# Kernel optimization log

Hardware: AMD Instinct MI355X
Metric: run time of the kernel (lower is better)

## Reference

```python
import jax, jax.numpy as jnp
import numpy as np

COUT, CIN = 1024, 1024  # self.shape = (cout, cin) in the torch module
NNZ = 131072


def setup_inputs() -> dict:
    key = jax.random.key(0)
    k_x, k_v, k_r, k_c = jax.random.split(key, 4)
    x = jax.random.normal(k_x, (4, 4096, CIN), dtype=jnp.float32)
    values = jax.random.normal(k_v, (NNZ,), dtype=jnp.float32)
    rows = jax.random.randint(k_r, (NNZ,), 0, COUT, dtype=jnp.int32)
    cols = jax.random.randint(k_c, (NNZ,), 0, CIN, dtype=jnp.int32)
    indices = jnp.stack([rows, cols], axis=0)  # [2, nnz], integer-valued
    return {"x": x, "values": values, "indices": indices}


def reference(x, values, indices):
    # torch: sparse_coo_tensor(indices, values, (cout, cin)).coalesce();
    # coalescing sums duplicate (row, col) entries -> scatter-add densify.
    rows, cols = indices[0], indices[1]
    W = jnp.zeros((COUT, CIN), dtype=values.dtype).at[rows, cols].add(values)
    # 3D path: out[b, l, co] = sum_ci W[co, ci] * x[b, l, ci]
    return jnp.einsum('blc,oc->blo', x, W)
```

## Files before the change

kernel.cpp:

```cpp
#include <hip/hip_runtime.h>
#include <cstdint>
#include <cstddef>

#define CIN  1024
#define COUT 1024

typedef __attribute__((ext_vector_type(8))) short bf16x8;
typedef __attribute__((ext_vector_type(4))) float f32x4;

__device__ __forceinline__ unsigned short f2bf(float f) {
    union { float f; unsigned int i; } v;
    v.f = f;
    unsigned int u = v.i;
    u += 0x7FFFu + ((u >> 16) & 1u);
    return (unsigned short)(u >> 16);
}

__global__ void zero_f32(float4* __restrict__ p) {
    p[blockIdx.x * 256 + threadIdx.x] = float4{0.f, 0.f, 0.f, 0.f};
}

__global__ void scatter_add(const float* __restrict__ vals,
                            const int* __restrict__ rows,
                            const int* __restrict__ cols,
                            float* __restrict__ W, int nnz) {
    int i = blockIdx.x * 256 + threadIdx.x;
    if (i < nnz) {
        atomicAdd(W + (size_t)rows[i] * CIN + cols[i], vals[i]);
    }
}

__global__ void cvt_bf16_bulk(const float* __restrict__ src, unsigned short* __restrict__ dst) {
    size_t i = ((size_t)blockIdx.x * 256 + threadIdx.x) * 8;
    float4 v0 = *(const float4*)(src + i);
    float4 v1 = *(const float4*)(src + i + 4);
    union { bf16x8 v; unsigned short u[8]; } w;
    w.u[0] = f2bf(v0.x); w.u[1] = f2bf(v0.y); w.u[2] = f2bf(v0.z); w.u[3] = f2bf(v0.w);
    w.u[4] = f2bf(v1.x); w.u[5] = f2bf(v1.y); w.u[6] = f2bf(v1.z); w.u[7] = f2bf(v1.w);
    *(bf16x8*)(dst + i) = w.v;
}

__global__ __launch_bounds__(256) void gemm_bt_bf16_sw(
    const unsigned short* __restrict__ A,
    const unsigned short* __restrict__ B,
    float* __restrict__ C,
    int M) {
    constexpr int K = CIN;
    constexpr int N = COUT;

    __shared__ __align__(16) unsigned short As[128 * 64];
    __shared__ __align__(16) unsigned short Bs[128 * 64];

    const int tid   = threadIdx.x;
    const int lane  = tid & 63;
    const int wave  = tid >> 6;
    const int waveM = (wave >> 1) * 64;
    const int waveN = (wave & 1) * 64;
    const int quad  = lane >> 4;
    const int l16   = lane & 15;

    const int rowA0 = blockIdx.x * 128;
    const int rowB0 = blockIdx.y * 128;

    const int stg_r  = tid >> 3;
    const int c_slot = tid & 7;
    const int c_data = c_slot ^ (stg_r & 7);
    const unsigned short* pa = A + (size_t)(rowA0 + stg_r) * K + c_data * 8;
    const unsigned short* pb = B + (size_t)(rowB0 + stg_r) * K + c_data * 8;
    const int ldsoff = tid * 8;

    f32x4 acc[4][4] = {};

    for (int k0 = 0; k0 < K; k0 += 64) {
#pragma unroll
        for (int it = 0; it < 4; ++it) {
            __builtin_amdgcn_global_load_lds(
                (const __attribute__((address_space(1))) void*)(pa + k0 + (size_t)it * 32 * K),
                (__attribute__((address_space(3))) void*)(As + it * 2048 + ldsoff),
                16, 0, 0);
            __builtin_amdgcn_global_load_lds(
                (const __attribute__((address_space(1))) void*)(pb + k0 + (size_t)it * 32 * K),
                (__attribute__((address_space(3))) void*)(Bs + it * 2048 + ldsoff),
                16, 0, 0);
        }
        __syncthreads();

        const int s7 = l16 & 7;
#pragma unroll
        for (int ks = 0; ks < 2; ++ks) {
            bf16x8 af[4], bfr[4];
            const int cx = ((ks * 4 + quad) ^ s7) * 8;
#pragma unroll
            for (int t = 0; t < 4; ++t) {
                af[t]  = *(const bf16x8*)(As + (waveM + t * 16 + l16) * 64 + cx);
                bfr[t] = *(const bf16x8*)(Bs + (waveN + t * 16 + l16) * 64 + cx);
            }
#pragma unroll
            for (int i = 0; i < 4; ++i)
#pragma unroll
                for (int j = 0; j < 4; ++j)
                    acc[i][j] = __builtin_amdgcn_mfma_f32_16x16x32_bf16(
                        af[i], bfr[j], acc[i][j], 0, 0, 0);
        }
        __syncthreads();
    }

#pragma unroll
    for (int i = 0; i < 4; ++i) {
#pragma unroll
        for (int r = 0; r < 4; ++r) {
            const int row = rowA0 + waveM + i * 16 + quad * 4 + r;
            float* cp = C + (size_t)row * N + rowB0 + waveN + l16;
#pragma unroll
            for (int j = 0; j < 4; ++j)
                cp[j * 16] = acc[i][j][r];
        }
    }
}

extern "C" void kernel_launch(void* const* d_in, const int* in_sizes, int n_in,
                              void* d_out, int out_size, void* d_ws, size_t ws_size,
                              hipStream_t stream) {
    const float* x    = (const float*)d_in[0];
    const float* vals = (const float*)d_in[1];
    const int*   idx  = (const int*)d_in[2];

    float* out = (float*)d_out;

    const int nnz = in_sizes[2] / 2;
    const int M   = in_sizes[0] / CIN;

    const size_t wf_bytes = (size_t)COUT * CIN * sizeof(float);
    const size_t wb_bytes = (size_t)COUT * CIN * sizeof(unsigned short);

    float*          Wf = (float*)d_ws;
    unsigned short* Wb = (unsigned short*)((char*)d_ws + wf_bytes);
    unsigned short* Xb = (unsigned short*)((char*)d_ws + wf_bytes + wb_bytes);

    zero_f32<<<dim3(COUT * CIN / (256 * 4)), dim3(256), 0, stream>>>((float4*)Wf);
    scatter_add<<<dim3((nnz + 255) / 256), dim3(256), 0, stream>>>(vals, idx, idx + nnz, Wf, nnz);
    cvt_bf16_bulk<<<dim3(COUT * CIN / (256 * 8)), dim3(256), 0, stream>>>(Wf, Wb);
    cvt_bf16_bulk<<<dim3((unsigned)((size_t)M * CIN / (256 * 8))), dim3(256), 0, stream>>>(x, Xb);
    gemm_bt_bf16_sw<<<dim3(M / 128, COUT / 128), dim3(256), 0, stream>>>(Xb, Wb, out, M);
}
```

Baseline: 161.7 us.

## Rewrite GEMM as 256x256 tile, 8-wave, double-buffered 8-phase pipelined kernel

Replaces the single-buffered 128x128 four-wave GEMM with a 256x256 tile computed by 8 waves. Each k-step is split into eight quadrant phases that interleave async global-to-LDS loads with MFMA work, using raw barriers, explicit vmcnt waits and setprio. Larger tiles raise data reuse per LDS load, and the double buffering hides memory latency behind compute. The cost is 128KB of LDS per block, fewer blocks (64 over the grid), and fragile hand-tuned waitcnt logic.

```diff
diff --git a/kernel.cpp b/kernel.cpp
--- a/kernel.cpp
+++ b/kernel.cpp
@@ -40,82 +40,132 @@
     *(bf16x8*)(dst + i) = w.v;
 }
 
-__global__ __launch_bounds__(256) void gemm_bt_bf16_sw(
+
+#define GLD16(SRC_, DST_)                                                     \
+  __builtin_amdgcn_global_load_lds(                                           \
+      (const __attribute__((address_space(1))) void*)(SRC_),                  \
+      (__attribute__((address_space(3))) void*)(DST_), 16, 0, 0)
+
+#define STAGE_A(BUF_, HALF_, KT_) do {                                        \
+    GLD16(pa + (size_t)((HALF_) * 128)      * CIN + (size_t)(KT_) * 64,       \
+          As + (BUF_) * 16384 + ((HALF_) * 128) * 64 + tid8);                 \
+    GLD16(pa + (size_t)((HALF_) * 128 + 64) * CIN + (size_t)(KT_) * 64,       \
+          As + (BUF_) * 16384 + ((HALF_) * 128 + 64) * 64 + tid8);            \
+  } while (0)
+
+#define STAGE_B(BUF_, HALF_, KT_) do {                                        \
+    GLD16(pb + (size_t)((HALF_) * 128)      * CIN + (size_t)(KT_) * 64,       \
+          Bs + (BUF_) * 16384 + ((HALF_) * 128) * 64 + tid8);                 \
+    GLD16(pb + (size_t)((HALF_) * 128 + 64) * CIN + (size_t)(KT_) * 64,       \
+          Bs + (BUF_) * 16384 + ((HALF_) * 128 + 64) * 64 + tid8);            \
+  } while (0)
+
+#define PHASE(BUF_, QA_, QB_, STAGE_BODY_, CKPT_BODY_) do {                   \
+    bf16x8 af[2][4];                                                          \
+    bf16x8 bfr[2][2];                                                         \
+    const unsigned short* abase_ =                                            \
+        As + (BUF_) * 16384 + ((QA_) * 128 + wm64) * 64;                      \
+    const unsigned short* bbase_ =                                            \
+        Bs + (BUF_) * 16384 + ((QB_) * 128 + wn32) * 64;                      \
+    _Pragma("unroll")                                                         \
+    for (int ks_ = 0; ks_ < 2; ++ks_) {                                       \
+      const int cx_ = ((ks_ * 4 + quad) ^ s7) * 8;                            \
+      _Pragma("unroll")                                                       \
+      for (int mf_ = 0; mf_ < 4; ++mf_)                                       \
+        af[ks_][mf_] = *(const bf16x8*)(abase_ + (mf_ * 16 + l16) * 64 + cx_);\
+      _Pragma("unroll")                                                       \
+      for (int nf_ = 0; nf_ < 2; ++nf_)                                       \
+        bfr[ks_][nf_] = *(const bf16x8*)(bbase_ + (nf_ * 16 + l16) * 64 + cx_);\
+    }                                                                         \
+    STAGE_BODY_                                                               \
+    __builtin_amdgcn_s_barrier();                                             \
+    asm volatile("s_waitcnt lgkmcnt(0)" ::: "memory");                        \
+    __builtin_amdgcn_sched_barrier(0);                                        \
+    __builtin_amdgcn_s_setprio(1);                                            \
+    _Pragma("unroll")                                                         \
+    for (int ks_ = 0; ks_ < 2; ++ks_)                                         \
+      _Pragma("unroll")                                                       \
+      for (int mf_ = 0; mf_ < 4; ++mf_)                                       \
+        _Pragma("unroll")                                                     \
+        for (int nf_ = 0; nf_ < 2; ++nf_)                                     \
+          acc[QA_][QB_][mf_][nf_] = __builtin_amdgcn_mfma_f32_16x16x32_bf16(  \
+              af[ks_][mf_], bfr[ks_][nf_], acc[QA_][QB_][mf_][nf_], 0, 0, 0); \
+    __builtin_amdgcn_s_setprio(0);                                            \
+    CKPT_BODY_                                                                \
+    __builtin_amdgcn_s_barrier();                                             \
+  } while (0)
+
+__global__ __launch_bounds__(512, 2) void gemm_8ph(
     const unsigned short* __restrict__ A,
     const unsigned short* __restrict__ B,
     float* __restrict__ C,
     int M) {
+    (void)M;
     constexpr int K = CIN;
-    constexpr int N = COUT;
 
-    __shared__ __align__(16) unsigned short As[128 * 64];
-    __shared__ __align__(16) unsigned short Bs[128 * 64];
+    __shared__ __align__(16) unsigned short As[2 * 16384];
+    __shared__ __align__(16) unsigned short Bs[2 * 16384];
 
-    const int tid   = threadIdx.x;
-    const int lane  = tid & 63;
-    const int wave  = tid >> 6;
-    const int waveM = (wave >> 1) * 64;
-    const int waveN = (wave & 1) * 64;
-    const int quad  = lane >> 4;
-    const int l16   = lane & 15;
+    const int tid  = threadIdx.x;
+    const int lane = tid & 63;
+    const int w    = tid >> 6;
+    const int quad = lane >> 4;
+    const int l16  = lane & 15;
+    const int s7   = l16 & 7;
+    const int wm64 = (w >> 2) * 64;
+    const int wn32 = (w & 3) * 32;
 
-    const int rowA0 = blockIdx.x * 128;
-    const int rowB0 = blockIdx.y * 128;
+    const int rowA0 = blockIdx.x * 256;
+    const int rowB0 = blockIdx.y * 256;
 
-    const int stg_r  = tid >> 3;
-    const int c_slot = tid & 7;
-    const int c_data = c_slot ^ (stg_r & 7);
-    const unsigned short* pa = A + (size_t)(rowA0 + stg_r) * K + c_data * 8;
-    const unsigned short* pb = B + (size_t)(rowB0 + stg_r) * K + c_data * 8;
-    const int ldsoff = tid * 8;
+    const int stg_row = tid >> 3;
+    const int c_data  = (tid & 7) ^ (stg_row & 7);
+    const int tid8    = tid * 8;
+    const unsigned short* pa = A + (size_t)(rowA0 + stg_row) * K + c_data * 8;
+    const unsigned short* pb = B + (size_t)(rowB0 + stg_row) * K + c_data * 8;
 
-    f32x4 acc[4][4] = {};
+    f32x4 acc[2][2][4][2] = {};
 
-    for (int k0 = 0; k0 < K; k0 += 64) {
-#pragma unroll
-        for (int it = 0; it < 4; ++it) {
-            __builtin_amdgcn_global_load_lds(
-                (const __attribute__((address_space(1))) void*)(pa + k0 + (size_t)it * 32 * K),
-                (__attribute__((address_space(3))) void*)(As + it * 2048 + ldsoff),
-                16, 0, 0);
-            __builtin_amdgcn_global_load_lds(
-                (const __attribute__((address_space(1))) void*)(pb + k0 + (size_t)it * 32 * K),
-                (__attribute__((address_space(3))) void*)(Bs + it * 2048 + ldsoff),
-                16, 0, 0);
-        }
-        __syncthreads();
+    STAGE_A(0, 0, 0); STAGE_A(0, 1, 0); STAGE_B(0, 0, 0); STAGE_B(0, 1, 0);
+    STAGE_A(1, 0, 1); STAGE_B(1, 0, 1);
+    asm volatile("s_waitcnt vmcnt(4)" ::: "memory");
+    __builtin_amdgcn_s_barrier();
 
-        const int s7 = l16 & 7;
-#pragma unroll
-        for (int ks = 0; ks < 2; ++ks) {
-            bf16x8 af[4], bfr[4];
-            const int cx = ((ks * 4 + quad) ^ s7) * 8;
-#pragma unroll
-            for (int t = 0; t < 4; ++t) {
-                af[t]  = *(const bf16x8*)(As + (waveM + t * 16 + l16) * 64 + cx);
-                bfr[t] = *(const bf16x8*)(Bs + (waveN + t * 16 + l16) * 64 + cx);
-            }
-#pragma unroll
-            for (int i = 0; i < 4; ++i)
-#pragma unroll
-                for (int j = 0; j < 4; ++j)
-                    acc[i][j] = __builtin_amdgcn_mfma_f32_16x16x32_bf16(
-                        af[i], bfr[j], acc[i][j], 0, 0, 0);
-        }
-        __syncthreads();
+#pragma unroll 1
+    for (int i = 0; i < 8; ++i) {
+        const int  k1 = 2 * i + 1;
+        const int  k2 = 2 * i + 2;
+        const int  k3 = 2 * i + 3;
+        const bool nl = (i < 7);
+
+        PHASE(0, 0, 0, STAGE_A(1, 1, k1); STAGE_B(1, 1, k1); , );
+        PHASE(0, 0, 1, , );
+        PHASE(0, 1, 0, if (nl) STAGE_A(0, 0, k2); , );
+        PHASE(0, 1, 1, if (nl) STAGE_B(0, 0, k2); ,
+              if (nl) { asm volatile("s_waitcnt vmcnt(4)" ::: "memory"); }
+              else    { asm volatile("s_waitcnt vmcnt(0)" ::: "memory"); } );
+        PHASE(1, 0, 0, if (nl) { STAGE_A(0, 1, k2); STAGE_B(0, 1, k2); } , );
+        PHASE(1, 0, 1, , );
+        PHASE(1, 1, 0, if (nl) STAGE_A(1, 0, k3); , );
+        PHASE(1, 1, 1, if (nl) STAGE_B(1, 0, k3); ,
+              if (nl) { asm volatile("s_waitcnt vmcnt(4)" ::: "memory"); } );
     }
 
 #pragma unroll
-    for (int i = 0; i < 4; ++i) {
+    for (int qa = 0; qa < 2; ++qa)
 #pragma unroll
-        for (int r = 0; r < 4; ++r) {
-            const int row = rowA0 + waveM + i * 16 + quad * 4 + r;
-            float* cp = C + (size_t)row * N + rowB0 + waveN + l16;
+        for (int qb = 0; qb < 2; ++qb)
 #pragma unroll
-            for (int j = 0; j < 4; ++j)
-                cp[j * 16] = acc[i][j][r];
-        }
-    }
+            for (int mf = 0; mf < 4; ++mf)
+#pragma unroll
+                for (int nf = 0; nf < 2; ++nf) {
+                    const int row0 = rowA0 + qa * 128 + wm64 + mf * 16 + quad * 4;
+                    float* cp = C + (size_t)row0 * COUT
+                                  + rowB0 + qb * 128 + wn32 + nf * 16 + l16;
+#pragma unroll
+                    for (int r = 0; r < 4; ++r)
+                        cp[(size_t)r * COUT] = acc[qa][qb][mf][nf][r];
+                }
 }
 
 extern "C" void kernel_launch(void* const* d_in, const int* in_sizes, int n_in,
@@ -141,5 +191,5 @@
     scatter_add<<<dim3((nnz + 255) / 256), dim3(256), 0, stream>>>(vals, idx, idx + nnz, Wf, nnz);
     cvt_bf16_bulk<<<dim3(COUT * CIN / (256 * 8)), dim3(256), 0, stream>>>(Wf, Wb);
     cvt_bf16_bulk<<<dim3((unsigned)((size_t)M * CIN / (256 * 8))), dim3(256), 0, stream>>>(x, Xb);
-    gemm_bt_bf16_sw<<<dim3(M / 128, COUT / 128), dim3(256), 0, stream>>>(Xb, Wb, out, M);
+    gemm_8ph<<<dim3(M / 256, COUT / 256), dim3(512), 0, stream>>>(Xb, Wb, out, M);
 }
```

After: 165.1 us. +2.1%, slower.

## Double-buffer GEMM with BK=32 stages and 256x128 tiles on 512-thread blocks

Applied to the files above, without the earlier changes.

Replaces the single-buffered BK=64 GEMM with a double-buffered BK=32 pipeline. The next K-slice is loaded into LDS via global_load_lds while MFMAs run on the current buffer, so each K step needs one barrier instead of two. The block tile grows to 256x128 with 8 waves (each still 64x64), and the XOR swizzle is adapted to 32-wide rows. This aims to hide global-load latency behind compute, at the cost of more LDS per block and a smaller grid.

```diff
diff --git a/kernel.cpp b/kernel.cpp
--- a/kernel.cpp
+++ b/kernel.cpp
@@ -40,82 +40,103 @@
     *(bf16x8*)(dst + i) = w.v;
 }
 
-__global__ __launch_bounds__(256) void gemm_bt_bf16_sw(
+
+#define GLD16(SRC_, DST_)                                                     \
+  __builtin_amdgcn_global_load_lds(                                           \
+      (const __attribute__((address_space(1))) void*)(SRC_),                  \
+      (__attribute__((address_space(3))) void*)(DST_), 16, 0, 0)
+
+__global__ __launch_bounds__(512, 4) void gemm_bk32(
     const unsigned short* __restrict__ A,
     const unsigned short* __restrict__ B,
     float* __restrict__ C,
     int M) {
+    (void)M;
     constexpr int K = CIN;
-    constexpr int N = COUT;
 
-    __shared__ __align__(16) unsigned short As[128 * 64];
-    __shared__ __align__(16) unsigned short Bs[128 * 64];
+    __shared__ __align__(16) unsigned short As[2 * 256 * 32];
+    __shared__ __align__(16) unsigned short Bs[2 * 128 * 32];
 
-    const int tid   = threadIdx.x;
-    const int lane  = tid & 63;
-    const int wave  = tid >> 6;
-    const int waveM = (wave >> 1) * 64;
-    const int waveN = (wave & 1) * 64;
-    const int quad  = lane >> 4;
-    const int l16   = lane & 15;
+    const int tid  = threadIdx.x;
+    const int lane = tid & 63;
+    const int w    = tid >> 6;
+    const int q    = lane >> 4;
+    const int l16  = lane & 15;
+    const int sR   = (l16 >> 1) & 3;
+    const int wm   = (w >> 1) * 64;
+    const int wn   = (w & 1) * 64;
 
-    const int rowA0 = blockIdx.x * 128;
+    const int rowA0 = blockIdx.x * 256;
     const int rowB0 = blockIdx.y * 128;
 
-    const int stg_r  = tid >> 3;
-    const int c_slot = tid & 7;
-    const int c_data = c_slot ^ (stg_r & 7);
-    const unsigned short* pa = A + (size_t)(rowA0 + stg_r) * K + c_data * 8;
-    const unsigned short* pb = B + (size_t)(rowB0 + stg_r) * K + c_data * 8;
-    const int ldsoff = tid * 8;
+    const int stg_row = tid >> 2;
+    const int c_data  = (tid & 3) ^ ((tid >> 3) & 3);
+    const int tid8    = tid * 8;
+    const unsigned short* pa = A + (size_t)(rowA0 + stg_row) * K + c_data * 8;
+    const unsigned short* pb = B + (size_t)(rowB0 + stg_row) * K + c_data * 8;
+
+    const int rslot8 = (q ^ sR) * 8;
 
     f32x4 acc[4][4] = {};
 
-    for (int k0 = 0; k0 < K; k0 += 64) {
-#pragma unroll
-        for (int it = 0; it < 4; ++it) {
-            __builtin_amdgcn_global_load_lds(
-                (const __attribute__((address_space(1))) void*)(pa + k0 + (size_t)it * 32 * K),
-                (__attribute__((address_space(3))) void*)(As + it * 2048 + ldsoff),
-                16, 0, 0);
-            __builtin_amdgcn_global_load_lds(
-                (const __attribute__((address_space(1))) void*)(pb + k0 + (size_t)it * 32 * K),
-                (__attribute__((address_space(3))) void*)(Bs + it * 2048 + ldsoff),
-                16, 0, 0);
+#define STAGE(BUF_, KT_) do {                                                 \
+    GLD16(pa + (KT_) * 32,                 As + (BUF_) * 8192 + tid8);        \
+    GLD16(pa + (size_t)128 * K + (KT_) * 32, As + (BUF_) * 8192 + 4096 + tid8); \
+    GLD16(pb + (KT_) * 32,                 Bs + (BUF_) * 4096 + tid8);        \
+  } while (0)
+
+#define BODY(BUF_) do {                                                       \
+    bf16x8 af[4], bfr[4];                                                     \
+    const unsigned short* ab_ = As + (BUF_) * 8192 + (wm + l16) * 32 + rslot8;\
+    const unsigned short* bb_ = Bs + (BUF_) * 4096 + (wn + l16) * 32 + rslot8;\
+    _Pragma("unroll")                                                         \
+    for (int mf_ = 0; mf_ < 4; ++mf_) af[mf_]  = *(const bf16x8*)(ab_ + mf_ * 512); \
+    _Pragma("unroll")                                                         \
+    for (int nf_ = 0; nf_ < 4; ++nf_) bfr[nf_] = *(const bf16x8*)(bb_ + nf_ * 512); \
+    _Pragma("unroll")                                                         \
+    for (int mf_ = 0; mf_ < 4; ++mf_)                                         \
+      _Pragma("unroll")                                                       \
+      for (int nf_ = 0; nf_ < 4; ++nf_)                                       \
+        acc[mf_][nf_] = __builtin_amdgcn_mfma_f32_16x16x32_bf16(              \
+            af[mf_], bfr[nf_], acc[mf_][nf_], 0, 0, 0);                       \
+  } while (0)
+
+#define ENDBAR() do {                                                         \
+    asm volatile("s_waitcnt vmcnt(0)" ::: "memory");                          \
+    __builtin_amdgcn_s_barrier();                                             \
+  } while (0)
+
+    STAGE(0, 0);
+    ENDBAR();
+
+#pragma unroll 1
+    for (int i = 0; i < 16; ++i) {
+        const int t0 = 2 * i;
+        STAGE(1, t0 + 1);
+        BODY(0);
+        ENDBAR();
+        if (i < 15) {
+            STAGE(0, t0 + 2);
+            BODY(1);
+            ENDBAR();
+        } else {
+            BODY(1);
         }
-        __syncthreads();
-
-        const int s7 = l16 & 7;
-#pragma unroll
-        for (int ks = 0; ks < 2; ++ks) {
-            bf16x8 af[4], bfr[4];
-            const int cx = ((ks * 4 + quad) ^ s7) * 8;
-#pragma unroll
-            for (int t = 0; t < 4; ++t) {
-                af[t]  = *(const bf16x8*)(As + (waveM + t * 16 + l16) * 64 + cx);
-                bfr[t] = *(const bf16x8*)(Bs + (waveN + t * 16 + l16) * 64 + cx);
-            }
-#pragma unroll
-            for (int i = 0; i < 4; ++i)
-#pragma unroll
-                for (int j = 0; j < 4; ++j)
-                    acc[i][j] = __builtin_amdgcn_mfma_f32_16x16x32_bf16(
-                        af[i], bfr[j], acc[i][j], 0, 0, 0);
-        }
-        __syncthreads();
     }
 
 #pragma unroll
-    for (int i = 0; i < 4; ++i) {
+    for (int mf = 0; mf < 4; ++mf)
 #pragma unroll
-        for (int r = 0; r < 4; ++r) {
-            const int row = rowA0 + waveM + i * 16 + quad * 4 + r;
-            float* cp = C + (size_t)row * N + rowB0 + waveN + l16;
+        for (int nf = 0; nf < 4; ++nf) {
+            const int row0 = rowA0 + wm + mf * 16 + q * 4;
+            float* cp = C + (size_t)row0 * COUT + rowB0 + wn + nf * 16 + l16;
 #pragma unroll
-            for (int j = 0; j < 4; ++j)
-                cp[j * 16] = acc[i][j][r];
+            for (int r = 0; r < 4; ++r)
+                cp[(size_t)r * COUT] = acc[mf][nf][r];
         }
-    }
+#undef STAGE
+#undef BODY
+#undef ENDBAR
 }
 
 extern "C" void kernel_launch(void* const* d_in, const int* in_sizes, int n_in,
@@ -141,5 +162,5 @@
     scatter_add<<<dim3((nnz + 255) / 256), dim3(256), 0, stream>>>(vals, idx, idx + nnz, Wf, nnz);
     cvt_bf16_bulk<<<dim3(COUT * CIN / (256 * 8)), dim3(256), 0, stream>>>(Wf, Wb);
     cvt_bf16_bulk<<<dim3((unsigned)((size_t)M * CIN / (256 * 8))), dim3(256), 0, stream>>>(x, Xb);
-    gemm_bt_bf16_sw<<<dim3(M / 128, COUT / 128), dim3(256), 0, stream>>>(Xb, Wb, out, M);
+    gemm_bk32<<<dim3(M / 256, COUT / 128), dim3(512), 0, stream>>>(Xb, Wb, out, M);
 }
```

After: 259.2 us. +60.3%, slower.
